# Optimization experiments

Hardware: AMD Instinct MI355X
Metric: run time of the kernel (lower is better)

The kernel has to match this reference:

```python
import jax, jax.numpy as jnp
import numpy as np

CHANNELS = 1024
PIVOT = 16384


def setup_inputs() -> dict:
    key = jax.random.key(0)
    k1, k2, k3 = jax.random.split(key, 3)
    x_Jx = jax.random.normal(k1, (3 * PIVOT, CHANNELS), dtype=jnp.float32)
    # Linear(channels, channels) params, torch-like init scale
    s = 1.0 / np.sqrt(CHANNELS)
    W = jax.random.uniform(k2, (CHANNELS, CHANNELS), dtype=jnp.float32, minval=-s, maxval=s)
    b = jax.random.uniform(k3, (CHANNELS,), dtype=jnp.float32, minval=-s, maxval=s)
    return {"x_Jx": x_Jx, "W": W, "b": b}


def reference(x_Jx, W, b):
    pivot = x_Jx.shape[0] // 3
    channels = W.shape[0]
    x = x_Jx[:pivot]                                   # [P, C]
    hAx = jnp.tanh(x @ W.T + b)                        # [P, C]
    hpAx = 1.0 - hAx ** 2                              # tanh'
    Jx = x_Jx[pivot:].reshape(pivot, channels, 2)      # [P, C, 2]
    # sum_j W[i,j] * Jx[p,j,k]  (the explicit broadcast-sum in torch is this GEMM)
    WJx = jnp.einsum('ij,pjk->pik', W, Jx)             # [P, C, 2]
    hpAJx = (hpAx[:, :, None] * WJx).reshape(-1, channels)  # [2P, C]
    return jnp.concatenate([hAx, hpAJx], axis=0)       # [3P, C]
```

## Files before the change

### kernel.cpp

```cpp
#include <hip/hip_runtime.h>
#include <hip/hip_bf16.h>
#include <cstdint>

typedef __attribute__((ext_vector_type(8))) short short8;
typedef __attribute__((ext_vector_type(4))) float floatx4;

__device__ __forceinline__ float tanh_fast(float x) {
    float e = __expf(2.0f * x);
    return 1.0f - 2.0f * __builtin_amdgcn_rcpf(e + 1.0f);
}

__device__ __forceinline__ unsigned int bf16_bits(float f) {
    __hip_bfloat16 h = __float2bfloat16(f);
    return (unsigned int)*reinterpret_cast<unsigned short*>(&h);
}
__device__ __forceinline__ unsigned int pack2(float lo, float hi) {
    return bf16_bits(lo) | (bf16_bits(hi) << 16);
}

#define LDS_STRIDE 72

__device__ __forceinline__ void swizzle_tile(int& row0, int& col0) {
    const int nwg  = gridDim.x * gridDim.y;
    const int flat = blockIdx.y * gridDim.x + blockIdx.x;
    const int swz  = (flat & 7) * (nwg >> 3) + (flat >> 3);
    col0 = (swz & 7) * 128;
    row0 = (swz >> 3) * 128;
}

__global__ __launch_bounds__(256) void k1_gemm_tanh(
    const float* __restrict__ X,
    const float* __restrict__ W,
    const float* __restrict__ Bv,
    float* __restrict__ out,
    int K)
{
    __shared__ __align__(16) short As[128 * LDS_STRIDE];
    __shared__ __align__(16) short Bs[128 * LDS_STRIDE];

    const int tid  = threadIdx.x;
    const int lane = tid & 63;
    const int wave = tid >> 6;
    const int wm = wave & 1, wn = wave >> 1;

    int row0, col0;
    swizzle_tile(row0, col0);

    const int l15  = lane & 15;
    const int quad = lane >> 4;
    const int a_base = (wm * 64 + l15) * LDS_STRIDE;
    const int b_base = (wn * 64 + l15) * LDS_STRIDE;

    floatx4 acc[4][4];
#pragma unroll
    for (int a = 0; a < 4; ++a)
#pragma unroll
        for (int b = 0; b < 4; ++b) acc[a][b] = (floatx4){0.f, 0.f, 0.f, 0.f};

    for (int k0 = 0; k0 < K; k0 += 64) {
        __syncthreads();
#pragma unroll
        for (int i = 0; i < 8; ++i) {
            const int g = i * 256 + tid;
            const int r = g >> 4, c = g & 15;
            const float4 va = *(const float4*)(X + (size_t)(row0 + r) * K + k0 + c * 4);
            const float4 vb = *(const float4*)(W + (size_t)(col0 + r) * K + k0 + c * 4);
            uint2 ea, eb;
            ea.x = pack2(va.x, va.y); ea.y = pack2(va.z, va.w);
            eb.x = pack2(vb.x, vb.y); eb.y = pack2(vb.z, vb.w);
            *(uint2*)&As[r * LDS_STRIDE + c * 4] = ea;
            *(uint2*)&Bs[r * LDS_STRIDE + c * 4] = eb;
        }
        __syncthreads();
#pragma unroll
        for (int ki = 0; ki < 2; ++ki) {
            const int kx = ki * 32 + quad * 8;
            short8 af[4], bf[4];
#pragma unroll
            for (int s = 0; s < 4; ++s)
                af[s] = *(const short8*)&As[a_base + s * 16 * LDS_STRIDE + kx];
#pragma unroll
            for (int s = 0; s < 4; ++s)
                bf[s] = *(const short8*)&Bs[b_base + s * 16 * LDS_STRIDE + kx];
#pragma unroll
            for (int a = 0; a < 4; ++a)
#pragma unroll
                for (int b = 0; b < 4; ++b)
                    acc[a][b] = __builtin_amdgcn_mfma_f32_16x16x32_bf16(
                        af[a], bf[b], acc[a][b], 0, 0, 0);
        }
    }

    float bv[4];
#pragma unroll
    for (int b = 0; b < 4; ++b)
        bv[b] = Bv[col0 + wn * 64 + b * 16 + l15];

#pragma unroll
    for (int a = 0; a < 4; ++a) {
        const int rbase = row0 + wm * 64 + a * 16 + quad * 4;
#pragma unroll
        for (int b = 0; b < 4; ++b) {
            const int n = col0 + wn * 64 + b * 16 + l15;
#pragma unroll
            for (int r = 0; r < 4; ++r)
                out[(size_t)(rbase + r) * 1024 + n] = tanh_fast(acc[a][b][r] + bv[b]);
        }
    }
}

__global__ __launch_bounds__(256) void k2_gemm_jac(
    const float* __restrict__ G,
    const float* __restrict__ W,
    const float* __restrict__ Hout,
    float* __restrict__ out2,
    int K)
{
    __shared__ __align__(16) short As[128 * LDS_STRIDE];
    __shared__ __align__(16) short Bs[128 * LDS_STRIDE];

    const int tid  = threadIdx.x;
    const int lane = tid & 63;
    const int wave = tid >> 6;
    const int wm = wave & 1, wn = wave >> 1;

    int r0, col0;
    swizzle_tile(r0, col0);
    const int p0 = r0 >> 1;

    const int l15  = lane & 15;
    const int quad = lane >> 4;
    const int a_base = (wm * 64 + l15) * LDS_STRIDE;
    const int b_base = (wn * 64 + l15) * LDS_STRIDE;

    floatx4 acc[4][4];
#pragma unroll
    for (int a = 0; a < 4; ++a)
#pragma unroll
        for (int b = 0; b < 4; ++b) acc[a][b] = (floatx4){0.f, 0.f, 0.f, 0.f};

    for (int k0 = 0; k0 < K; k0 += 64) {
        __syncthreads();
#pragma unroll
        for (int i = 0; i < 8; ++i) {
            const int g = i * 256 + tid;
            const int r = g >> 4, c = g & 15;
            const float4 vb = *(const float4*)(W + (size_t)(col0 + r) * K + k0 + c * 4);
            uint2 eb;
            eb.x = pack2(vb.x, vb.y); eb.y = pack2(vb.z, vb.w);
            *(uint2*)&Bs[r * LDS_STRIDE + c * 4] = eb;
        }
#pragma unroll
        for (int i = 0; i < 4; ++i) {
            const int g = i * 256 + tid;
            const int q = g >> 4, d = g & 15;
            const float* src = G + (size_t)(p0 + q) * 2048 + 2 * k0 + d * 8;
            const float4 u0 = *(const float4*)src;
            const float4 u1 = *(const float4*)(src + 4);
            uint2 E, O;
            E.x = pack2(u0.x, u0.z); E.y = pack2(u1.x, u1.z);
            O.x = pack2(u0.y, u0.w); O.y = pack2(u1.y, u1.w);
            *(uint2*)&As[(2 * q)     * LDS_STRIDE + d * 4] = E;
            *(uint2*)&As[(2 * q + 1) * LDS_STRIDE + d * 4] = O;
        }
        __syncthreads();
#pragma unroll
        for (int ki = 0; ki < 2; ++ki) {
            const int kx = ki * 32 + quad * 8;
            short8 af[4], bf[4];
#pragma unroll
            for (int s = 0; s < 4; ++s)
                af[s] = *(const short8*)&As[a_base + s * 16 * LDS_STRIDE + kx];
#pragma unroll
            for (int s = 0; s < 4; ++s)
                bf[s] = *(const short8*)&Bs[b_base + s * 16 * LDS_STRIDE + kx];
#pragma unroll
            for (int a = 0; a < 4; ++a)
#pragma unroll
                for (int b = 0; b < 4; ++b)
                    acc[a][b] = __builtin_amdgcn_mfma_f32_16x16x32_bf16(
                        af[a], bf[b], acc[a][b], 0, 0, 0);
        }
    }

#pragma unroll
    for (int a = 0; a < 4; ++a) {
        const int rb = r0 + wm * 64 + a * 16 + quad * 4;
#pragma unroll
        for (int b = 0; b < 4; ++b) {
            const int i = col0 + wn * 64 + b * 16 + l15;
            const int shift = (i >= 512) ? 1 : 0;
            const int ccol = 2 * i - shift * 1024;
#pragma unroll
            for (int pr = 0; pr < 2; ++pr) {
                const int re = rb + pr * 2;
                const int p  = re >> 1;
                const float h  = Hout[(size_t)p * 1024 + i];
                const float hp = 1.0f - h * h;
                float2 st;
                st.x = hp * acc[a][b][pr * 2];
                st.y = hp * acc[a][b][pr * 2 + 1];
                *(float2*)&out2[(size_t)(re + shift) * 1024 + ccol] = st;
            }
        }
    }
}

extern "C" void kernel_launch(void* const* d_in, const int* in_sizes, int n_in,
                              void* d_out, int out_size, void* d_ws, size_t ws_size,
                              hipStream_t stream) {
    const float* xJx = (const float*)d_in[0];
    const float* W   = (const float*)d_in[1];
    const float* bv  = (const float*)d_in[2];
    float* out = (float*)d_out;

    const int C     = 1024;
    const int rows3 = in_sizes[0] / C;
    const int pivot = rows3 / 3;

    dim3 blk(256);
    dim3 g1(C / 128, pivot / 128);
    k1_gemm_tanh<<<g1, blk, 0, stream>>>(xJx, W, bv, out, C);

    dim3 g2(C / 128, (2 * pivot) / 128);
    k2_gemm_jac<<<g2, blk, 0, stream>>>(xJx + (size_t)pivot * C, W, out,
                                        out + (size_t)pivot * C, C);
}
```

Baseline: 526.3 us.

## Pre-convert operands to bf16 and stage GEMM tiles via direct global-to-LDS loads

```diff
diff --git a/kernel.cpp b/kernel.cpp
--- a/kernel.cpp
+++ b/kernel.cpp
@@ -18,7 +18,11 @@
     return bf16_bits(lo) | (bf16_bits(hi) << 16);
 }
 
-#define LDS_STRIDE 72
+__device__ __forceinline__ void async16(const void* g, void* l) {
+    __builtin_amdgcn_global_load_lds(
+        (const __attribute__((address_space(1))) unsigned int*)g,
+        (__attribute__((address_space(3))) unsigned int*)l, 16, 0, 0);
+}
 
 __device__ __forceinline__ void swizzle_tile(int& row0, int& col0) {
     const int nwg  = gridDim.x * gridDim.y;
@@ -28,15 +32,96 @@
     row0 = (swz >> 3) * 128;
 }
 
-__global__ __launch_bounds__(256) void k1_gemm_tanh(
-    const float* __restrict__ X,
+
+__global__ __launch_bounds__(256) void cvt_prep(
+    const float* __restrict__ X, const float* __restrict__ G,
     const float* __restrict__ W,
+    short* __restrict__ Xb, short* __restrict__ Mb, short* __restrict__ Wb,
+    int nbX, int nbG)
+{
+    const int tid = threadIdx.x;
+    const int b   = blockIdx.x;
+    if (b < nbX) {
+        const size_t e = ((size_t)b * 256 + tid) * 16;
+        const float4 f0 = *(const float4*)(X + e);
+        const float4 f1 = *(const float4*)(X + e + 4);
+        const float4 f2 = *(const float4*)(X + e + 8);
+        const float4 f3 = *(const float4*)(X + e + 12);
+        uint4 o0, o1;
+        o0.x = pack2(f0.x, f0.y); o0.y = pack2(f0.z, f0.w);
+        o0.z = pack2(f1.x, f1.y); o0.w = pack2(f1.z, f1.w);
+        o1.x = pack2(f2.x, f2.y); o1.y = pack2(f2.z, f2.w);
+        o1.z = pack2(f3.x, f3.y); o1.w = pack2(f3.z, f3.w);
+        *(uint4*)(Xb + e)     = o0;
+        *(uint4*)(Xb + e + 8) = o1;
+    } else if (b < nbX + nbG) {
+        const size_t s = (size_t)(b - nbX) * 256 + tid;
+        const size_t p = s >> 7;
+        const int    c = (int)(s & 127);
+        const float* src = G + p * 2048 + (size_t)c * 16;
+        const float4 f0 = *(const float4*)(src);
+        const float4 f1 = *(const float4*)(src + 4);
+        const float4 f2 = *(const float4*)(src + 8);
+        const float4 f3 = *(const float4*)(src + 12);
+        uint4 E, O;
+        E.x = pack2(f0.x, f0.z); E.y = pack2(f1.x, f1.z);
+        E.z = pack2(f2.x, f2.z); E.w = pack2(f3.x, f3.z);
+        O.x = pack2(f0.y, f0.w); O.y = pack2(f1.y, f1.w);
+        O.z = pack2(f2.y, f2.w); O.w = pack2(f3.y, f3.w);
+        *(uint4*)(Mb + (2 * p)     * 1024 + (size_t)c * 8) = E;
+        *(uint4*)(Mb + (2 * p + 1) * 1024 + (size_t)c * 8) = O;
+    } else {
+        const size_t e = ((size_t)(b - nbX - nbG) * 256 + tid) * 16;
+        const float4 f0 = *(const float4*)(W + e);
+        const float4 f1 = *(const float4*)(W + e + 4);
+        const float4 f2 = *(const float4*)(W + e + 8);
+        const float4 f3 = *(const float4*)(W + e + 12);
+        uint4 o0, o1;
+        o0.x = pack2(f0.x, f0.y); o0.y = pack2(f0.z, f0.w);
+        o0.z = pack2(f1.x, f1.y); o0.w = pack2(f1.z, f1.w);
+        o1.x = pack2(f2.x, f2.y); o1.y = pack2(f2.z, f2.w);
+        o1.z = pack2(f3.x, f3.y); o1.w = pack2(f3.z, f3.w);
+        *(uint4*)(Wb + e)     = o0;
+        *(uint4*)(Wb + e + 8) = o1;
+    }
+}
+
+#define GEMM_STAGE_AND_MMA(Ag, Bg)                                             \
+    for (int k0 = 0; k0 < K; k0 += 64) {                                       \
+        __syncthreads();                                                       \
+        _Pragma("unroll")                                                      \
+        for (int i = 0; i < 4; ++i) {                                          \
+            async16(Ag + (size_t)i * 8 * K + k0, Al + i * 512);                \
+            async16(Bg + (size_t)i * 8 * K + k0, Bl + i * 512);                \
+        }                                                                      \
+        __syncthreads();                                                       \
+        _Pragma("unroll")                                                      \
+        for (int ki = 0; ki < 2; ++ki) {                                       \
+            const int kx = ki * 32 + quad * 8;                                 \
+            short8 af[4], bf[4];                                               \
+            _Pragma("unroll")                                                  \
+            for (int s = 0; s < 4; ++s)                                        \
+                af[s] = *(const short8*)&As[a_base + s * 16 * 64 + kx];        \
+            _Pragma("unroll")                                                  \
+            for (int s = 0; s < 4; ++s)                                        \
+                bf[s] = *(const short8*)&Bs[b_base + s * 16 * 64 + kx];        \
+            _Pragma("unroll")                                                  \
+            for (int a = 0; a < 4; ++a)                                        \
+                _Pragma("unroll")                                              \
+                for (int b = 0; b < 4; ++b)                                    \
+                    acc[a][b] = __builtin_amdgcn_mfma_f32_16x16x32_bf16(       \
+                        af[a], bf[b], acc[a][b], 0, 0, 0);                     \
+        }                                                                      \
+    }
+
+__global__ __launch_bounds__(256) void k1b_gemm_tanh(
+    const short* __restrict__ A,
+    const short* __restrict__ B,
     const float* __restrict__ Bv,
-    float* __restrict__ out,
-    int K)
+    float* __restrict__ out, int K)
 {
-    __shared__ __align__(16) short As[128 * LDS_STRIDE];
-    __shared__ __align__(16) short Bs[128 * LDS_STRIDE];
+    __shared__ __align__(16) short As[128 * 64];
+    __shared__ __align__(16) short Bs[128 * 64];
 
     const int tid  = threadIdx.x;
     const int lane = tid & 63;
@@ -46,6 +131,118 @@
     int row0, col0;
     swizzle_tile(row0, col0);
 
+    const int l15  = lane & 15;
+    const int quad = lane >> 4;
+    const int a_base = (wm * 64 + l15) * 64;
+    const int b_base = (wn * 64 + l15) * 64;
+
+    const int lrow = lane >> 3;
+    const int lcol = lane & 7;
+    const short* Ag = A + (size_t)(row0 + wave * 32 + lrow) * K + lcol * 8;
+    const short* Bg = B + (size_t)(col0 + wave * 32 + lrow) * K + lcol * 8;
+    short* Al = As + wave * 32 * 64;
+    short* Bl = Bs + wave * 32 * 64;
+
+    floatx4 acc[4][4];
+#pragma unroll
+    for (int a = 0; a < 4; ++a)
+#pragma unroll
+        for (int b = 0; b < 4; ++b) acc[a][b] = (floatx4){0.f, 0.f, 0.f, 0.f};
+
+    GEMM_STAGE_AND_MMA(Ag, Bg)
+
+    float bv[4];
+#pragma unroll
+    for (int b = 0; b < 4; ++b)
+        bv[b] = Bv[col0 + wn * 64 + b * 16 + l15];
+
+#pragma unroll
+    for (int a = 0; a < 4; ++a) {
+        const int rbase = row0 + wm * 64 + a * 16 + quad * 4;
+#pragma unroll
+        for (int b = 0; b < 4; ++b) {
+            const int n = col0 + wn * 64 + b * 16 + l15;
+#pragma unroll
+            for (int r = 0; r < 4; ++r)
+                out[(size_t)(rbase + r) * 1024 + n] = tanh_fast(acc[a][b][r] + bv[b]);
+        }
+    }
+}
+
+__global__ __launch_bounds__(256) void k2b_gemm_jac(
+    const short* __restrict__ A,
+    const short* __restrict__ B,
+    const float* __restrict__ Hout,
+    float* __restrict__ out2, int K)
+{
+    __shared__ __align__(16) short As[128 * 64];
+    __shared__ __align__(16) short Bs[128 * 64];
+
+    const int tid  = threadIdx.x;
+    const int lane = tid & 63;
+    const int wave = tid >> 6;
+    const int wm = wave & 1, wn = wave >> 1;
+
+    int r0, col0;
+    swizzle_tile(r0, col0);
+
+    const int l15  = lane & 15;
+    const int quad = lane >> 4;
+    const int a_base = (wm * 64 + l15) * 64;
+    const int b_base = (wn * 64 + l15) * 64;
+
+    const int lrow = lane >> 3;
+    const int lcol = lane & 7;
+    const short* Ag = A + (size_t)(r0 + wave * 32 + lrow) * K + lcol * 8;
+    const short* Bg = B + (size_t)(col0 + wave * 32 + lrow) * K + lcol * 8;
+    short* Al = As + wave * 32 * 64;
+    short* Bl = Bs + wave * 32 * 64;
+
+    floatx4 acc[4][4];
+#pragma unroll
+    for (int a = 0; a < 4; ++a)
+#pragma unroll
+        for (int b = 0; b < 4; ++b) acc[a][b] = (floatx4){0.f, 0.f, 0.f, 0.f};
+
+    GEMM_STAGE_AND_MMA(Ag, Bg)
+
+#pragma unroll
+    for (int a = 0; a < 4; ++a) {
+        const int rb = r0 + wm * 64 + a * 16 + quad * 4;
+#pragma unroll
+        for (int b = 0; b < 4; ++b) {
+            const int i = col0 + wn * 64 + b * 16 + l15;
+            const int shift = (i >= 512) ? 1 : 0;
+            const int ccol = 2 * i - shift * 1024;
+#pragma unroll
+            for (int pr = 0; pr < 2; ++pr) {
+                const int re = rb + pr * 2;
+                const int p  = re >> 1;
+                const float h  = Hout[(size_t)p * 1024 + i];
+                const float hp = 1.0f - h * h;
+                float2 st;
+                st.x = hp * acc[a][b][pr * 2];
+                st.y = hp * acc[a][b][pr * 2 + 1];
+                *(float2*)&out2[(size_t)(re + shift) * 1024 + ccol] = st;
+            }
+        }
+    }
+}
+
+#define LDS_STRIDE 72
+
+__global__ __launch_bounds__(256) void k1_gemm_tanh(
+    const float* __restrict__ X, const float* __restrict__ W,
+    const float* __restrict__ Bv, float* __restrict__ out, int K)
+{
+    __shared__ __align__(16) short As[128 * LDS_STRIDE];
+    __shared__ __align__(16) short Bs[128 * LDS_STRIDE];
+    const int tid  = threadIdx.x;
+    const int lane = tid & 63;
+    const int wave = tid >> 6;
+    const int wm = wave & 1, wn = wave >> 1;
+    int row0, col0;
+    swizzle_tile(row0, col0);
     const int l15  = lane & 15;
     const int quad = lane >> 4;
     const int a_base = (wm * 64 + l15) * LDS_STRIDE;
@@ -95,7 +292,6 @@
 #pragma unroll
     for (int b = 0; b < 4; ++b)
         bv[b] = Bv[col0 + wn * 64 + b * 16 + l15];
-
 #pragma unroll
     for (int a = 0; a < 4; ++a) {
         const int rbase = row0 + wm * 64 + a * 16 + quad * 4;
@@ -110,24 +306,18 @@
 }
 
 __global__ __launch_bounds__(256) void k2_gemm_jac(
-    const float* __restrict__ G,
-    const float* __restrict__ W,
-    const float* __restrict__ Hout,
-    float* __restrict__ out2,
-    int K)
+    const float* __restrict__ G, const float* __restrict__ W,
+    const float* __restrict__ Hout, float* __restrict__ out2, int K)
 {
     __shared__ __align__(16) short As[128 * LDS_STRIDE];
     __shared__ __align__(16) short Bs[128 * LDS_STRIDE];
-
     const int tid  = threadIdx.x;
     const int lane = tid & 63;
     const int wave = tid >> 6;
     const int wm = wave & 1, wn = wave >> 1;
-
     int r0, col0;
     swizzle_tile(r0, col0);
     const int p0 = r0 >> 1;
-
     const int l15  = lane & 15;
     const int quad = lane >> 4;
     const int a_base = (wm * 64 + l15) * LDS_STRIDE;
@@ -218,11 +408,33 @@
     const int rows3 = in_sizes[0] / C;
     const int pivot = rows3 / 3;
 
+    const size_t szXb = (size_t)pivot * C * 2;
+    const size_t szMb = (size_t)2 * pivot * C * 2;
+    const size_t szWb = (size_t)C * C * 2;
     dim3 blk(256);
-    dim3 g1(C / 128, pivot / 128);
-    k1_gemm_tanh<<<g1, blk, 0, stream>>>(xJx, W, bv, out, C);
-
-    dim3 g2(C / 128, (2 * pivot) / 128);
-    k2_gemm_jac<<<g2, blk, 0, stream>>>(xJx + (size_t)pivot * C, W, out,
-                                        out + (size_t)pivot * C, C);
-}
+
+    if (ws_size >= szXb + szMb + szWb) {
+        short* Xb = (short*)d_ws;
+        short* Mb = (short*)((char*)d_ws + szXb);
+        short* Wb = (short*)((char*)d_ws + szXb + szMb);
+
+        const int nbX = (pivot * C) / 4096;
+        const int nbG = (pivot * 2 * C) / 4096;
+        const int nbW = (C * C) / 4096;
+        cvt_prep<<<dim3(nbX + nbG + nbW), blk, 0, stream>>>(
+            xJx, xJx + (size_t)pivot * C, W, Xb, Mb, Wb, nbX, nbG);
+
+        dim3 g1(C / 128, pivot / 128);
+        k1b_gemm_tanh<<<g1, blk, 0, stream>>>(Xb, Wb, bv, out, C);
+
+        dim3 g2(C / 128, (2 * pivot) / 128);
+        k2b_gemm_jac<<<g2, blk, 0, stream>>>(Mb, Wb, out,
+                                             out + (size_t)pivot * C, C);
+    } else {
+        dim3 g1(C / 128, pivot / 128);
+        k1_gemm_tanh<<<g1, blk, 0, stream>>>(xJx, W, bv, out, C);
+        dim3 g2(C / 128, (2 * pivot) / 128);
+        k2_gemm_jac<<<g2, blk, 0, stream>>>(xJx + (size_t)pivot * C, W, out,
+                                            out + (size_t)pivot * C, C);
+    }
+}
```

New measurement: 520.3 us. About the same (-1.1%).
